# Kernel tuning notes

Measured on AMD Instinct MI355X. Metric: run time of the kernel, lower is better.

The kernel has to match this reference:

```python
import jax, jax.numpy as jnp
import numpy as np

B, S, D, H = 4, 1024, 1024, 16
DK = D // H


def setup_inputs() -> dict:
    key = jax.random.key(0)
    ks = jax.random.split(key, 8)
    scale = 1.0 / np.sqrt(D)
    inp = {
        "x": jax.random.normal(ks[0], (B, S, D), jnp.float32),
        "encoder_output": jax.random.normal(ks[1], (B, S, D), jnp.float32),
        "src_mask": jnp.ones((1, 1, 1, S), jnp.int32),
        "tgt_mask": jnp.tril(jnp.ones((S, S), jnp.int32))[None, None, :, :],
        "wq_self": jax.random.normal(ks[2], (D, D), jnp.float32) * scale,
        "wk_self": jax.random.normal(ks[3], (D, D), jnp.float32) * scale,
        "wv_self": jax.random.normal(ks[4], (D, D), jnp.float32) * scale,
        "wq_cross": jax.random.normal(ks[5], (D, D), jnp.float32) * scale,
        "wk_cross": jax.random.normal(ks[6], (D, D), jnp.float32) * scale,
        "wv_cross": jax.random.normal(ks[7], (D, D), jnp.float32) * scale,
    }
    return inp


def _mha(q_in, k_in, v_in, wq, wk, wv, mask):
    # nn.Linear (no bias): y = x @ W.T
    def split_heads(t):
        b, s, _ = t.shape
        return t.reshape(b, s, H, DK).transpose(0, 2, 1, 3)  # [B,H,S,DK]

    q = split_heads(q_in @ wq.T)
    k = split_heads(k_in @ wk.T)
    v = split_heads(v_in @ wv.T)
    scores = jnp.einsum("bhqd,bhkd->bhqk", q, k) / jnp.sqrt(jnp.float32(DK))
    scores = jnp.where(mask == 0, jnp.float32(-1e9), scores)
    attn = jax.nn.softmax(scores, axis=-1)
    out = jnp.einsum("bhqk,bhkd->bhqd", attn, v)  # [B,H,S,DK]
    return out.transpose(0, 2, 1, 3).reshape(q_in.shape[0], -1, H * DK)


def reference(x, encoder_output, src_mask, tgt_mask,
              wq_self, wk_self, wv_self, wq_cross, wk_cross, wv_cross):
    x = _mha(x, x, x, wq_self, wk_self, wv_self, tgt_mask)
    x = _mha(x, encoder_output, encoder_output, wq_cross, wk_cross, wv_cross, src_mask)
    return x
```

## Files before the change

### kernel.cpp

```cpp
#include <hip/hip_runtime.h>
#include <stdint.h>


typedef unsigned short u16;
typedef short b16x8 __attribute__((ext_vector_type(8)));
typedef short b16x4 __attribute__((ext_vector_type(4)));
typedef float f32x4 __attribute__((ext_vector_type(4)));

__device__ __forceinline__ u16 f2bf(float f) {
  union { float f; uint32_t u; } v; v.f = f;
  uint32_t r = v.u + 0x7fffu + ((v.u >> 16) & 1u);
  return (u16)(r >> 16);
}

__device__ __forceinline__ f32x4 mfma16(b16x8 a, b16x8 b, f32x4 c) {
  return __builtin_amdgcn_mfma_f32_16x16x32_bf16(a, b, c, 0, 0, 0);
}

__device__ __forceinline__ void gld16(const void* g, void* l) {
  __builtin_amdgcn_global_load_lds(
      (const __attribute__((address_space(1))) void*)g,
      (__attribute__((address_space(3))) void*)l, 16, 0, 0);
}

__device__ __forceinline__ float ex2(float x) {
  float r; asm("v_exp_f32 %0, %1" : "=v"(r) : "v"(x)); return r;
}

__device__ __forceinline__ uint32_t cvtpk(float a, float b) {
  uint32_t r;
  asm("v_cvt_pk_bf16_f32 %0, %1, %2" : "=v"(r) : "v"(a), "v"(b));
  return r;
}

__global__ __launch_bounds__(256) void k_cvt2(const float* __restrict__ a,
                                              const float* __restrict__ b,
                                              u16* __restrict__ oa,
                                              u16* __restrict__ ob) {
  const float* in = blockIdx.y ? b : a;
  u16* out = blockIdx.y ? ob : oa;
  int i = (blockIdx.x * 256 + threadIdx.x) * 8;
  float4 x = *(const float4*)(in + i);
  float4 y = *(const float4*)(in + i + 4);
  b16x8 v;
  v[0] = (short)f2bf(x.x); v[1] = (short)f2bf(x.y);
  v[2] = (short)f2bf(x.z); v[3] = (short)f2bf(x.w);
  v[4] = (short)f2bf(y.x); v[5] = (short)f2bf(y.y);
  v[6] = (short)f2bf(y.z); v[7] = (short)f2bf(y.w);
  *(b16x8*)(out + i) = v;
}

__global__ __launch_bounds__(256) void k_cvtw(
    const float* __restrict__ w0, const float* __restrict__ w1,
    const float* __restrict__ w2, const float* __restrict__ w3,
    const float* __restrict__ w4, const float* __restrict__ w5,
    u16* __restrict__ wsc, u16* __restrict__ wcc) {
  const int idx = blockIdx.y;
  const float* in;
  switch (idx) {
    case 0: in = w0; break; case 1: in = w1; break; case 2: in = w2; break;
    case 3: in = w3; break; case 4: in = w4; break; default: in = w5; break;
  }
  u16* out = (idx < 3 ? wsc : wcc) + (idx % 3) * 1048576;
  const float sc = (idx % 3 == 0) ? 0.18033688f : 1.0f;
  int i = (blockIdx.x * 256 + threadIdx.x) * 8;
  float4 x = *(const float4*)(in + i);
  float4 y = *(const float4*)(in + i + 4);
  b16x8 v;
  v[0] = (short)f2bf(x.x * sc); v[1] = (short)f2bf(x.y * sc);
  v[2] = (short)f2bf(x.z * sc); v[3] = (short)f2bf(x.w * sc);
  v[4] = (short)f2bf(y.x * sc); v[5] = (short)f2bf(y.y * sc);
  v[6] = (short)f2bf(y.z * sc); v[7] = (short)f2bf(y.w * sc);
  *(b16x8*)(out + i) = v;
}

__global__ __launch_bounds__(256) void k_gemm_bt(const u16* __restrict__ A,
                                                 const u16* __restrict__ B,
                                                 u16* __restrict__ C,
                                                 int M, int N, int K) {
  __shared__ u16 Ab[128 * 32];
  __shared__ u16 Bb[128 * 32];
  const int tid = threadIdx.x;
  const int lane = tid & 63, w = tid >> 6;
  const int wr = w >> 1, wc = w & 1;
  const int q = lane & 15, hi = lane >> 4;
  const int nwg = gridDim.x * gridDim.y;
  const int id = blockIdx.y * gridDim.x + blockIdx.x;
  const int swz = (id & 7) * (nwg >> 3) + (id >> 3);
  const int bx = swz % gridDim.x, by = swz / gridDim.x;
  const int mbase = by * 128, nbase = bx * 128;
  f32x4 acc[4][4] = {};
  for (int kb = 0; kb < K; kb += 32) {
    __syncthreads();
#pragma unroll
    for (int r = 0; r < 2; ++r) {
      int c = tid + 256 * r;
      int row = c >> 2, ch = c & 3;
      gld16(&A[(size_t)(mbase + row) * K + kb + ch * 8], &Ab[c * 8]);
      gld16(&B[(size_t)(nbase + row) * K + kb + ch * 8], &Bb[c * 8]);
    }
    __syncthreads();
    b16x8 af[4], bf[4];
#pragma unroll
    for (int mi = 0; mi < 4; ++mi)
      af[mi] = *(const b16x8*)&Ab[(wr * 64 + mi * 16 + q) * 32 + hi * 8];
#pragma unroll
    for (int ni = 0; ni < 4; ++ni)
      bf[ni] = *(const b16x8*)&Bb[(wc * 64 + ni * 16 + q) * 32 + hi * 8];
#pragma unroll
    for (int mi = 0; mi < 4; ++mi)
#pragma unroll
      for (int ni = 0; ni < 4; ++ni)
        acc[mi][ni] = mfma16(af[mi], bf[ni], acc[mi][ni]);
  }
#pragma unroll
  for (int mi = 0; mi < 4; ++mi)
#pragma unroll
    for (int ni = 0; ni < 4; ++ni) {
      int m0 = mbase + wr * 64 + mi * 16 + hi * 4;
      int n0 = nbase + wc * 64 + ni * 16 + q;
#pragma unroll
      for (int i = 0; i < 4; ++i)
        C[(size_t)(m0 + i) * N + n0] = f2bf(acc[mi][ni][i]);
    }
}

__global__ __launch_bounds__(256) void k_vt(const u16* __restrict__ in, int sIn,
                                            int coff, u16* __restrict__ out) {
  __shared__ u16 T[64 * 72];
  const int tid = threadIdx.x;
  const int bh = blockIdx.y, kb = blockIdx.x * 64;
  const int b = bh >> 4, h = bh & 15;
  const int kvp = tid >> 3, ch = tid & 7;
  const u16* p = in + (size_t)(b * 1024 + kb + 2 * kvp) * sIn + coff + h * 64 + ch * 8;
  b16x8 r0 = *(const b16x8*)p;
  b16x8 r1 = *(const b16x8*)(p + sIn);
#pragma unroll
  for (int j = 0; j < 8; ++j) {
    int i = (j + ch) & 7;
    uint32_t pk = (uint32_t)(u16)r0[i] | ((uint32_t)(u16)r1[i] << 16);
    *(uint32_t*)&T[(ch * 8 + i) * 72 + 2 * kvp] = pk;
  }
  __syncthreads();
  const int d = tid >> 2, seg = tid & 3;
  b16x8 v0 = *(const b16x8*)&T[d * 72 + seg * 16];
  b16x8 v1 = *(const b16x8*)&T[d * 72 + seg * 16 + 8];
  u16* o = out + (size_t)(bh * 64 + d) * 1024 + kb + seg * 16;
  *(b16x8*)o = v0;
  *(b16x8*)(o + 8) = v1;
}

template <int CAUSAL, typename OT>
__global__ __launch_bounds__(256, 3) void attn4(
    const u16* __restrict__ Qp, int sQ,
    const u16* __restrict__ Kp, int sK, int koff,
    const u16* __restrict__ Vt,
    OT* __restrict__ Op, int sO) {
  __shared__ u16 Ksh[2][64 * 64];
  __shared__ u16 Vsh[2][64 * 64];
  __shared__ u16 Plds[4][32 * 72];
  const int tid = threadIdx.x;
  const int lane = tid & 63, w = tid >> 6;
  const int lq = lane & 15, hi = lane >> 4;

  const int id = blockIdx.y * gridDim.x + blockIdx.x;
  const int xcd = id & 7, l = id >> 3;
  const int bh = xcd * 8 + (l >> 3);
  const int qb = (l < 32) ? (l & 7) : 7 - (l & 7);

  const size_t rowb = (size_t)(bh >> 4) * 1024;
  const int h = bh & 15;
  const int qw0 = qb * 128 + w * 32;
  const int nt = CAUSAL ? 2 * qb + 2 : 16;

  const u16* Kbase = Kp + rowb * (size_t)sK + koff + h * 64;
  const u16* Vbase = Vt + (size_t)bh * 65536;
  const u16* Qb = Qp + (rowb + qw0 + lq) * (size_t)sQ + h * 64 + hi * 8;
  u16* Pw = &Plds[w][0];

  b16x8 qf[2][2];
  qf[0][0] = *(const b16x8*)Qb;
  qf[0][1] = *(const b16x8*)(Qb + 32);
  qf[1][0] = *(const b16x8*)(Qb + (size_t)16 * sQ);
  qf[1][1] = *(const b16x8*)(Qb + (size_t)16 * sQ + 32);

  b16x8 ones;
#pragma unroll
  for (int i = 0; i < 8; ++i) ones[i] = (short)0x3F80;

  const int key = lq & 7;

  f32x4 acc[2][4] = {};
  f32x4 accl[2] = {};
  float m0 = -1e30f, m1 = -1e30f;

  auto stage = [&](int bf, int kt2) {
    const int kb2 = kt2 * 64;
#pragma unroll
    for (int r = 0; r < 2; ++r) {
      int c = tid + 256 * r;
      int row = c >> 3, ch = c & 7;
      int sw = row & 7;
      gld16(&Kbase[(size_t)(kb2 + row) * sK + ((ch ^ sw) << 3)],
            &Ksh[bf][c * 8]);
      gld16(&Vbase[(size_t)row * 1024 + kb2 + ((ch ^ sw) << 3)],
            &Vsh[bf][c * 8]);
    }
  };

  stage(0, 0);
  for (int kt = 0; kt < nt; ++kt) {
    __syncthreads();
    if (kt + 1 < nt) stage((kt + 1) & 1, kt + 1);
    const int kb = kt * 64;
    if (CAUSAL && kb > qw0 + 31) continue;
    const u16* Kl = Ksh[kt & 1];
    const u16* Vl = Vsh[kt & 1];

    f32x4 st[2][4];
#pragma unroll
    for (int t = 0; t < 4; ++t) {
      const int row = 16 * t + lq;
      b16x8 k0 = *(const b16x8*)&Kl[row * 64 + ((hi ^ key) << 3)];
      b16x8 k1 = *(const b16x8*)&Kl[row * 64 + (((4 + hi) ^ key) << 3)];
      f32x4 z0 = {}, z1 = {};
      z0 = mfma16(k0, qf[0][0], z0);
      st[0][t] = mfma16(k1, qf[0][1], z0);
      z1 = mfma16(k0, qf[1][0], z1);
      st[1][t] = mfma16(k1, qf[1][1], z1);
    }

    const bool dm = CAUSAL && (kb + 63 > qw0);
    float pm[2];
#pragma unroll
    for (int g = 0; g < 2; ++g) {
      if (dm) {
        const int qg = qw0 + g * 16 + lq;
#pragma unroll
        for (int t = 0; t < 4; ++t)
#pragma unroll
          for (int i = 0; i < 4; ++i)
            if (kb + 16 * t + 4 * hi + i > qg) st[g][t][i] = -INFINITY;
      }
      float m = -INFINITY;
#pragma unroll
      for (int t = 0; t < 4; ++t)
#pragma unroll
        for (int i = 0; i < 4; ++i) m = fmaxf(m, st[g][t][i]);
      m = fmaxf(m, __shfl_xor(m, 16));
      m = fmaxf(m, __shfl_xor(m, 32));
      pm[g] = m;
    }

    if (!__all((pm[0] <= m0 + 10.f) && (pm[1] <= m1 + 10.f))) {
      float n0 = fmaxf(m0, pm[0]), n1 = fmaxf(m1, pm[1]);
      float f0 = ex2(m0 - n0), f1 = ex2(m1 - n1);
#pragma unroll
      for (int t = 0; t < 4; ++t)
#pragma unroll
        for (int i = 0; i < 4; ++i) {
          acc[0][t][i] *= f0;
          acc[1][t][i] *= f1;
        }
#pragma unroll
      for (int i = 0; i < 4; ++i) { accl[0][i] *= f0; accl[1][i] *= f1; }
      m0 = n0; m1 = n1;
    }

#pragma unroll
    for (int g = 0; g < 2; ++g) {
      const float mm = g ? m1 : m0;
#pragma unroll
      for (int t = 0; t < 4; ++t) {
        uint2 pw;
        pw.x = cvtpk(ex2(st[g][t][0] - mm), ex2(st[g][t][1] - mm));
        pw.y = cvtpk(ex2(st[g][t][2] - mm), ex2(st[g][t][3] - mm));
        *(uint2*)&Pw[(g * 16 + lq) * 72 + 16 * t + 4 * hi] = pw;
      }
    }

    b16x8 av0[4], av1[4];
#pragma unroll
    for (int t = 0; t < 4; ++t) {
      const int rv = 16 * t + lq;
      av0[t] = *(const b16x8*)&Vl[rv * 64 + ((hi ^ key) << 3)];
      av1[t] = *(const b16x8*)&Vl[rv * 64 + (((4 + hi) ^ key) << 3)];
    }

#pragma unroll
    for (int g = 0; g < 2; ++g) {
      b16x8 bp0 = *(const b16x8*)&Pw[(g * 16 + lq) * 72 + hi * 8];
      b16x8 bp1 = *(const b16x8*)&Pw[(g * 16 + lq) * 72 + 32 + hi * 8];
      accl[g] = mfma16(ones, bp0, accl[g]);
      accl[g] = mfma16(ones, bp1, accl[g]);
#pragma unroll
      for (int t = 0; t < 4; ++t) {
        acc[g][t] = mfma16(av0[t], bp0, acc[g][t]);
        acc[g][t] = mfma16(av1[t], bp1, acc[g][t]);
      }
    }
  }

#pragma unroll
  for (int g = 0; g < 2; ++g) {
    const float inv = 1.0f / accl[g][0];
    const size_t ob = (rowb + qw0 + g * 16 + lq) * (size_t)sO + h * 64;
#pragma unroll
    for (int t = 0; t < 4; ++t) {
      const int d = 16 * t + 4 * hi;
      if constexpr (sizeof(OT) == 2) {
        b16x4 o;
        o[0] = (short)f2bf(acc[g][t][0] * inv);
        o[1] = (short)f2bf(acc[g][t][1] * inv);
        o[2] = (short)f2bf(acc[g][t][2] * inv);
        o[3] = (short)f2bf(acc[g][t][3] * inv);
        *(b16x4*)&((u16*)Op)[ob + d] = o;
      } else {
        float4 o = make_float4(acc[g][t][0] * inv, acc[g][t][1] * inv,
                               acc[g][t][2] * inv, acc[g][t][3] * inv);
        *(float4*)&((float*)Op)[ob + d] = o;
      }
    }
  }
}

extern "C" void kernel_launch(void* const* d_in, const int* in_sizes, int n_in,
                              void* d_out, int out_size, void* d_ws, size_t ws_size,
                              hipStream_t stream) {
  (void)in_sizes; (void)n_in; (void)out_size; (void)ws_size;
  const float* x   = (const float*)d_in[0];
  const float* enc = (const float*)d_in[1];
  const float* wqs = (const float*)d_in[4];
  const float* wks = (const float*)d_in[5];
  const float* wvs = (const float*)d_in[6];
  const float* wqc = (const float*)d_in[7];
  const float* wkc = (const float*)d_in[8];
  const float* wvc = (const float*)d_in[9];

  u16* ws   = (u16*)d_ws;
  u16* xb   = ws;
  u16* encb = ws + 4194304;
  u16* wsc  = ws + 8388608;
  u16* wcc  = ws + 11534336;
  u16* qkv1 = ws + 14680064;
  u16* x1b  = ws + 27262976;
  u16* q2   = ws + 31457280;
  u16* kv2  = ws + 35651584;

  k_cvt2<<<dim3(2048, 2), 256, 0, stream>>>(x, enc, xb, encb);
  k_cvtw<<<dim3(512, 6), 256, 0, stream>>>(wqs, wks, wvs, wqc, wkc, wvc,
                                           wsc, wcc);

  k_gemm_bt<<<dim3(24, 32), 256, 0, stream>>>(xb, wsc, qkv1, 4096, 3072, 1024);
  k_vt<<<dim3(16, 64), 256, 0, stream>>>(qkv1, 3072, 2048, xb);
  attn4<1, u16><<<dim3(8, 64), 256, 0, stream>>>(
      qkv1, 3072, qkv1, 3072, 1024, xb, x1b, 1024);

  k_gemm_bt<<<dim3(8, 32), 256, 0, stream>>>(x1b, wcc, q2, 4096, 1024, 1024);
  k_gemm_bt<<<dim3(16, 32), 256, 0, stream>>>(encb, wcc + 1048576, kv2,
                                              4096, 2048, 1024);
  k_vt<<<dim3(16, 64), 256, 0, stream>>>(kv2, 2048, 1024, encb);
  attn4<0, float><<<dim3(8, 64), 256, 0, stream>>>(
      q2, 1024, kv2, 2048, 0, encb, (float*)d_out, 1024);
}
```

Before: 268.8 us.

## Merge conversion kernels, batch cross-attn GEMMs, vectorize GEMM epilogue stores

Combines the activation and weight fp32-to-bf16 conversions into a single launch. The cross-attention Q projection and the KV projection now run as one grouped GEMM launch that picks its operands per column tile, so two launches become one and the larger grid fills the device better. The GEMM swaps the MFMA operands so each lane holds four consecutive output columns, which lets the epilogue use packed bf16 conversion and 8-byte stores instead of scalar 2-byte stores. K is now hardcoded to 1024.

Result: slower. 280.2 us (+4.2%).

```diff
diff --git a/kernel.cpp b/kernel.cpp
--- a/kernel.cpp
+++ b/kernel.cpp
@@ -33,51 +33,48 @@
   return r;
 }
 
-__global__ __launch_bounds__(256) void k_cvt2(const float* __restrict__ a,
-                                              const float* __restrict__ b,
-                                              u16* __restrict__ oa,
-                                              u16* __restrict__ ob) {
-  const float* in = blockIdx.y ? b : a;
-  u16* out = blockIdx.y ? ob : oa;
-  int i = (blockIdx.x * 256 + threadIdx.x) * 8;
-  float4 x = *(const float4*)(in + i);
-  float4 y = *(const float4*)(in + i + 4);
-  b16x8 v;
-  v[0] = (short)f2bf(x.x); v[1] = (short)f2bf(x.y);
-  v[2] = (short)f2bf(x.z); v[3] = (short)f2bf(x.w);
-  v[4] = (short)f2bf(y.x); v[5] = (short)f2bf(y.y);
-  v[6] = (short)f2bf(y.z); v[7] = (short)f2bf(y.w);
-  *(b16x8*)(out + i) = v;
-}
-
-__global__ __launch_bounds__(256) void k_cvtw(
+__global__ __launch_bounds__(256) void k_cvt_all(
+    const float* __restrict__ x, const float* __restrict__ enc,
     const float* __restrict__ w0, const float* __restrict__ w1,
     const float* __restrict__ w2, const float* __restrict__ w3,
     const float* __restrict__ w4, const float* __restrict__ w5,
+    u16* __restrict__ xb, u16* __restrict__ encb,
     u16* __restrict__ wsc, u16* __restrict__ wcc) {
-  const int idx = blockIdx.y;
+  const int id = blockIdx.x;
   const float* in;
-  switch (idx) {
-    case 0: in = w0; break; case 1: in = w1; break; case 2: in = w2; break;
-    case 3: in = w3; break; case 4: in = w4; break; default: in = w5; break;
-  }
-  u16* out = (idx < 3 ? wsc : wcc) + (idx % 3) * 1048576;
-  const float sc = (idx % 3 == 0) ? 0.18033688f : 1.0f;
-  int i = (blockIdx.x * 256 + threadIdx.x) * 8;
-  float4 x = *(const float4*)(in + i);
-  float4 y = *(const float4*)(in + i + 4);
+  u16* out;
+  float sc = 1.0f;
+  int off;
+  if (id < 2048) {
+    in = x; out = xb; off = id;
+  } else if (id < 4096) {
+    in = enc; out = encb; off = id - 2048;
+  } else {
+    const int wi = (id - 4096) >> 9;
+    off = (id - 4096) & 511;
+    switch (wi) {
+      case 0: in = w0; break; case 1: in = w1; break; case 2: in = w2; break;
+      case 3: in = w3; break; case 4: in = w4; break; default: in = w5; break;
+    }
+    out = (wi < 3 ? wsc : wcc) + (wi % 3) * 1048576;
+    if (wi % 3 == 0) sc = 0.18033688f;
+  }
+  const int i = (off * 256 + threadIdx.x) * 8;
+  float4 a = *(const float4*)(in + i);
+  float4 b = *(const float4*)(in + i + 4);
   b16x8 v;
-  v[0] = (short)f2bf(x.x * sc); v[1] = (short)f2bf(x.y * sc);
-  v[2] = (short)f2bf(x.z * sc); v[3] = (short)f2bf(x.w * sc);
-  v[4] = (short)f2bf(y.x * sc); v[5] = (short)f2bf(y.y * sc);
-  v[6] = (short)f2bf(y.z * sc); v[7] = (short)f2bf(y.w * sc);
+  v[0] = (short)f2bf(a.x * sc); v[1] = (short)f2bf(a.y * sc);
+  v[2] = (short)f2bf(a.z * sc); v[3] = (short)f2bf(a.w * sc);
+  v[4] = (short)f2bf(b.x * sc); v[5] = (short)f2bf(b.y * sc);
+  v[6] = (short)f2bf(b.z * sc); v[7] = (short)f2bf(b.w * sc);
   *(b16x8*)(out + i) = v;
 }
 
-__global__ __launch_bounds__(256) void k_gemm_bt(const u16* __restrict__ A,
-                                                 const u16* __restrict__ B,
-                                                 u16* __restrict__ C,
-                                                 int M, int N, int K) {
+__global__ __launch_bounds__(256) void k_gemm_bt(
+    const u16* __restrict__ A0, const u16* __restrict__ B0,
+    u16* __restrict__ C0, int N0, int nbx0,
+    const u16* __restrict__ A1, const u16* __restrict__ B1,
+    u16* __restrict__ C1, int N1) {
   __shared__ u16 Ab[128 * 32];
   __shared__ u16 Bb[128 * 32];
   const int tid = threadIdx.x;
@@ -88,16 +85,19 @@
   const int id = blockIdx.y * gridDim.x + blockIdx.x;
   const int swz = (id & 7) * (nwg >> 3) + (id >> 3);
   const int bx = swz % gridDim.x, by = swz / gridDim.x;
-  const int mbase = by * 128, nbase = bx * 128;
+  const u16* A; const u16* B; u16* C; int N, nb;
+  if (bx < nbx0) { A = A0; B = B0; C = C0; N = N0; nb = bx; }
+  else           { A = A1; B = B1; C = C1; N = N1; nb = bx - nbx0; }
+  const int mbase = by * 128, nbase = nb * 128;
   f32x4 acc[4][4] = {};
-  for (int kb = 0; kb < K; kb += 32) {
+  for (int kb = 0; kb < 1024; kb += 32) {
     __syncthreads();
 #pragma unroll
     for (int r = 0; r < 2; ++r) {
       int c = tid + 256 * r;
       int row = c >> 2, ch = c & 3;
-      gld16(&A[(size_t)(mbase + row) * K + kb + ch * 8], &Ab[c * 8]);
-      gld16(&B[(size_t)(nbase + row) * K + kb + ch * 8], &Bb[c * 8]);
+      gld16(&A[(size_t)(mbase + row) * 1024 + kb + ch * 8], &Ab[c * 8]);
+      gld16(&B[(size_t)(nbase + row) * 1024 + kb + ch * 8], &Bb[c * 8]);
     }
     __syncthreads();
     b16x8 af[4], bf[4];
@@ -111,18 +111,20 @@
     for (int mi = 0; mi < 4; ++mi)
 #pragma unroll
       for (int ni = 0; ni < 4; ++ni)
-        acc[mi][ni] = mfma16(af[mi], bf[ni], acc[mi][ni]);
-  }
-#pragma unroll
-  for (int mi = 0; mi < 4; ++mi)
+        acc[mi][ni] = mfma16(bf[ni], af[mi], acc[mi][ni]);
+  }
+#pragma unroll
+  for (int mi = 0; mi < 4; ++mi) {
+    const int m = mbase + wr * 64 + mi * 16 + q;
 #pragma unroll
     for (int ni = 0; ni < 4; ++ni) {
-      int m0 = mbase + wr * 64 + mi * 16 + hi * 4;
-      int n0 = nbase + wc * 64 + ni * 16 + q;
-#pragma unroll
-      for (int i = 0; i < 4; ++i)
-        C[(size_t)(m0 + i) * N + n0] = f2bf(acc[mi][ni][i]);
-    }
+      const int nc = nbase + wc * 64 + ni * 16 + hi * 4;
+      uint2 o;
+      o.x = cvtpk(acc[mi][ni][0], acc[mi][ni][1]);
+      o.y = cvtpk(acc[mi][ni][2], acc[mi][ni][3]);
+      *(uint2*)&C[(size_t)m * N + nc] = o;
+    }
+  }
 }
 
 __global__ __launch_bounds__(256) void k_vt(const u16* __restrict__ in, int sIn,
@@ -347,18 +349,17 @@
   u16* q2   = ws + 31457280;
   u16* kv2  = ws + 35651584;
 
-  k_cvt2<<<dim3(2048, 2), 256, 0, stream>>>(x, enc, xb, encb);
-  k_cvtw<<<dim3(512, 6), 256, 0, stream>>>(wqs, wks, wvs, wqc, wkc, wvc,
-                                           wsc, wcc);
-
-  k_gemm_bt<<<dim3(24, 32), 256, 0, stream>>>(xb, wsc, qkv1, 4096, 3072, 1024);
+  k_cvt_all<<<7168, 256, 0, stream>>>(x, enc, wqs, wks, wvs, wqc, wkc, wvc,
+                                      xb, encb, wsc, wcc);
+
+  k_gemm_bt<<<dim3(24, 32), 256, 0, stream>>>(xb, wsc, qkv1, 3072, 24,
+                                              xb, wsc, qkv1, 3072);
   k_vt<<<dim3(16, 64), 256, 0, stream>>>(qkv1, 3072, 2048, xb);
   attn4<1, u16><<<dim3(8, 64), 256, 0, stream>>>(
       qkv1, 3072, qkv1, 3072, 1024, xb, x1b, 1024);
 
-  k_gemm_bt<<<dim3(8, 32), 256, 0, stream>>>(x1b, wcc, q2, 4096, 1024, 1024);
-  k_gemm_bt<<<dim3(16, 32), 256, 0, stream>>>(encb, wcc + 1048576, kv2,
-                                              4096, 2048, 1024);
+  k_gemm_bt<<<dim3(24, 32), 256, 0, stream>>>(x1b, wcc, q2, 1024, 8,
+                                              encb, wcc + 1048576, kv2, 2048);
   k_vt<<<dim3(16, 64), 256, 0, stream>>>(kv2, 2048, 1024, encb);
   attn4<0, float><<<dim3(8, 64), 256, 0, stream>>>(
       q2, 1024, kv2, 2048, 0, encb, (float*)d_out, 1024);
```
